# Kernel tuning notes

Hardware: AMD Instinct MI355X
Metric: run time of the kernel (lower is better)

Reference implementation:

```python
import jax, jax.numpy as jnp
import numpy as np

B, T, J, E, H = 32, 120, 24, 128, 8
d = E // H           # attention_dim = 16
D = J * E            # input_dim = 3072
FF = 256
NEG = -1e9


def _bn(x, g, b):
    # BatchNorm1d over channels-last layout: normalize each of D channels over (batch, time)
    m = x.mean(axis=(0, 1))
    v = x.var(axis=(0, 1))
    return (x - m) * jax.lax.rsqrt(v + 1e-5) * g + b


def setup_inputs() -> dict:
    key = jax.random.key(0)
    ks = jax.random.split(key, 12)
    s = 0.05  # keep activations well-scaled
    return {
        "src_seqs": jax.random.normal(ks[0], (B, T, D), jnp.float32),
        "Wq_t": jax.random.normal(ks[1], (H, J, d, E), jnp.float32) * s,
        "Wk_t": jax.random.normal(ks[2], (H, J, d, E), jnp.float32) * s,
        "Wv_t": jax.random.normal(ks[3], (H, J, d, E), jnp.float32) * s,
        "Wp_t": jax.random.normal(ks[4], (D, D), jnp.float32) * s,
        "bp_t": jnp.zeros((D,), jnp.float32),
        "g_t": jnp.ones((D,), jnp.float32),
        "b_t": jnp.zeros((D,), jnp.float32),
        "Wq_s": jax.random.normal(ks[5], (H, J, d, E), jnp.float32) * s,
        "Wk_s": jax.random.normal(ks[6], (H, d, E), jnp.float32) * s,
        "Wv_s": jax.random.normal(ks[7], (H, d, E), jnp.float32) * s,
        "Wp_s": jax.random.normal(ks[8], (D, D), jnp.float32) * s,
        "bp_s": jnp.zeros((D,), jnp.float32),
        "g_s": jnp.ones((D,), jnp.float32),
        "b_s": jnp.zeros((D,), jnp.float32),
        "W1": jax.random.normal(ks[9], (FF, D), jnp.float32) * s,
        "b1": jnp.zeros((FF,), jnp.float32),
        "W2": jax.random.normal(ks[10], (D, FF), jnp.float32) * s,
        "b2": jnp.zeros((D,), jnp.float32),
        "g_f": jnp.ones((D,), jnp.float32),
        "b_f": jnp.zeros((D,), jnp.float32),
    }


def reference(src_seqs, Wq_t, Wk_t, Wv_t, Wp_t, bp_t, g_t, b_t,
              Wq_s, Wk_s, Wv_s, Wp_s, bp_s, g_s, b_s,
              W1, b1, W2, b2, g_f, b_f):
    Bz, Tz, Dz = src_seqs.shape
    x = src_seqs.reshape(Bz, Tz, J, E)  # per-joint embeddings
    sc = 1.0 / jnp.sqrt(jnp.float32(d))

    # ---- temporal attention (per head h, per joint j; causal over time) ----
    q = jnp.einsum('btje,hjde->bhjtd', x, Wq_t)
    k = jnp.einsum('btje,hjde->bhjtd', x, Wk_t)
    v = jnp.einsum('btje,hjde->bhjtd', x, Wv_t)
    causal = jnp.where(jnp.tril(jnp.ones((Tz, Tz), bool)), 0.0, NEG)
    a = jax.nn.softmax(jnp.einsum('bhjtd,bhjsd->bhjts', q, k) * sc + causal, axis=-1)
    ta = jnp.einsum('bhjts,bhjsd->bhjtd', a, v)
    # concat order: heads outer, joints inner -> (b,t,h,j,d)
    ta = ta.transpose(0, 3, 1, 2, 4).reshape(Bz, Tz, Dz)
    ta = ta @ Wp_t.T + bp_t
    ta = _bn(ta + src_seqs, g_t, b_t)  # dropout=identity (eval)

    # ---- spatial attention (per head h; attends over joints, shared K/V proj) ----
    qs = jnp.einsum('btje,hjde->bhtjd', x, Wq_s)
    ks = jnp.einsum('btje,hde->bhtjd', x, Wk_s)
    vs = jnp.einsum('btje,hde->bhtjd', x, Wv_s)
    asft = jax.nn.softmax(jnp.einsum('bhtjd,bhtkd->bhtjk', qs, ks) * sc, axis=-1)
    sa = jnp.einsum('bhtjk,bhtkd->bhtjd', asft, vs)
    sa = sa.transpose(0, 2, 1, 3, 4).reshape(Bz, Tz, Dz)  # (b,t,h,j,d)
    sa = sa @ Wp_s.T + bp_s
    sa = _bn(sa + src_seqs, g_s, b_s)

    # ---- feed-forward + residual + norm ----
    att = ta + sa
    h1 = jax.nn.relu(att @ W1.T + b1)
    out = _bn((h1 @ W2.T + b2) + att, g_f, b_f)
    return out
```

## Files before the change

### kernel.cpp

```cpp
#include <hip/hip_runtime.h>

typedef unsigned short u16;
typedef __bf16 bf16x8 __attribute__((ext_vector_type(8)));
typedef float f4 __attribute__((ext_vector_type(4)));
typedef float float4v __attribute__((ext_vector_type(4)));
typedef u16 u16x4 __attribute__((ext_vector_type(4)));

#define NX 11796480
#define LDP 136

__device__ __forceinline__ float bf2f(u16 u){ __bf16 h = __builtin_bit_cast(__bf16, u); return (float)h; }
__device__ __forceinline__ u16 f2bf(float f){ __bf16 h = (__bf16)f; return __builtin_bit_cast(u16, h); }

__device__ __forceinline__ void gload_lds16(const u16* g, u16* l){
  __builtin_amdgcn_global_load_lds((const __attribute__((address_space(1))) void*)g,
                                   (__attribute__((address_space(3))) void*)l, 16, 0, 0);
}

__device__ __forceinline__ void cvt4seg(const float* __restrict__ in, u16* __restrict__ out, int i){
  float4v v = *(const float4v*)&in[i*4];
  u16x4 o;
  o[0]=f2bf(v[0]); o[1]=f2bf(v[1]); o[2]=f2bf(v[2]); o[3]=f2bf(v[3]);
  *(u16x4*)&out[i*4] = o;
}

__global__ void k_prep(const float* __restrict__ src, u16* __restrict__ x_bf,
                       const float* __restrict__ wpt, u16* __restrict__ wptb,
                       const float* __restrict__ wps, u16* __restrict__ wpsb,
                       const float* __restrict__ w1,  u16* __restrict__ w1b,
                       const float* __restrict__ w2,  u16* __restrict__ w2b,
                       const float* __restrict__ wqt, const float* __restrict__ wkt,
                       const float* __restrict__ wvt, const float* __restrict__ wqs,
                       const float* __restrict__ wks, const float* __restrict__ wvs,
                       u16* __restrict__ wcat, float* __restrict__ accs){
  int i = blockIdx.x*256 + threadIdx.x;
  if (i < 18432){ accs[i] = 0.f; return; }
  i -= 18432;
  if (i < 2949120){ cvt4seg(src, x_bf, i); return; }
  i -= 2949120;
  if (i < 2359296){ cvt4seg(wpt, wptb, i); return; }
  i -= 2359296;
  if (i < 2359296){ cvt4seg(wps, wpsb, i); return; }
  i -= 2359296;
  if (i < 196608){ cvt4seg(w1, w1b, i); return; }
  i -= 196608;
  if (i < 196608){ cvt4seg(w2, w2b, i); return; }
  i -= 196608;
  int e = i & 127;
  int n = (i >> 7) % 768;
  int j = i / (768*128);
  float v;
  if (n < 512){
    int tn = n >> 7, hh = (n >> 4) & 7, dd = n & 15;
    const float* W = (tn==0)? wqt : (tn==1)? wkt : (tn==2)? wvt : wqs;
    v = W[(((hh*24 + j)*16 + dd) << 7) + e];
  } else {
    int m = n - 512;
    int tn = m >> 7, hh = (m >> 4) & 7, dd = m & 15;
    const float* W = (tn==0)? wks : wvs;
    v = W[((hh*16 + dd) << 7) + e];
  }
  wcat[i] = f2bf(v);
}

__device__ __forceinline__ void stageQB(const u16* __restrict__ Bb, u16* __restrict__ dst,
                                        int tid, int srow16, int gcol){
  #pragma unroll
  for (int it=0; it<4; it++){
    int row = srow16 + it*16;
    gload_lds16(&Bb[(size_t)row*128 + gcol], dst + tid*8 + it*2048);
  }
}

__global__ __launch_bounds__(256)
void gemm_qkv(const u16* __restrict__ x, const u16* __restrict__ wcat,
              u16* __restrict__ qt, u16* __restrict__ kt, u16* __restrict__ vt,
              u16* __restrict__ qs, u16* __restrict__ ks, u16* __restrict__ vs)
{
  __shared__ __align__(16) u16 smem[32768];
  u16* As  = smem;
  u16* Bs0 = smem + 16384;
  u16* Bs1 = smem + 24576;
  int m0 = blockIdx.x*128, j = blockIdx.y;
  const u16* Ab = x + (size_t)m0*3072 + j*128;
  const u16* Bbase = wcat + (size_t)j*98304;
  int tid = threadIdx.x, lane = tid & 63, wid = tid >> 6;
  int quad = lane >> 4, r16 = lane & 15;
  int srow16 = tid >> 4;
  int cslot  = tid & 15;
  int gcol   = (cslot ^ srow16) * 8;

  #pragma unroll
  for (int it=0; it<8; it++){
    int row = srow16 + it*16;
    gload_lds16(&Ab[(size_t)row*3072 + gcol], As + tid*8 + it*2048);
  }
  stageQB(Bbase,            Bs0, tid, srow16, gcol);
  stageQB(Bbase + 64*128,   Bs1, tid, srow16, gcol);
  asm volatile("s_waitcnt vmcnt(4)" ::: "memory");
  __builtin_amdgcn_s_barrier();

  for (int nc=0; nc<12; nc++){
    const u16* Bc = (nc & 1) ? Bs1 : Bs0;

    f4 acc[2][4];
    #pragma unroll
    for (int mt=0; mt<2; mt++)
      #pragma unroll
      for (int nt=0; nt<4; nt++)
        #pragma unroll
        for (int q=0; q<4; q++) acc[mt][nt][q] = 0.f;

    #pragma unroll
    for (int kk=0; kk<4; kk++){
      const int soff = ((kk*4 + quad) ^ r16) * 8;
      bf16x8 af[2], bfr[4];
      #pragma unroll
      for (int mt=0; mt<2; mt++)
        af[mt] = *(const bf16x8*)&As[(wid*32 + mt*16 + r16)*128 + soff];
      #pragma unroll
      for (int nt=0; nt<4; nt++)
        bfr[nt] = *(const bf16x8*)&Bc[(nt*16 + r16)*128 + soff];
      #pragma unroll
      for (int mt=0; mt<2; mt++)
        #pragma unroll
        for (int nt=0; nt<4; nt++)
          acc[mt][nt] = __builtin_amdgcn_mfma_f32_16x16x32_bf16(af[mt], bfr[nt], acc[mt][nt], 0, 0, 0);
    }

    #pragma unroll
    for (int mt=0; mt<2; mt++){
      #pragma unroll
      for (int reg=0; reg<4; reg++){
        int row = m0 + wid*32 + mt*16 + quad*4 + reg;
        int b = row / 120, t = row % 120;
        #pragma unroll
        for (int nt=0; nt<4; nt++){
          int n = nc*64 + nt*16 + r16;
          u16 uv = f2bf(acc[mt][nt][reg]);
          if (n < 384){
            int tn = n >> 7, hh = (n >> 4) & 7, dd = n & 15;
            u16* base = (tn==0)? qt : (tn==1)? kt : vt;
            base[((((size_t)(b*8+hh)*24 + j)*120 + t) << 4) + dd] = uv;
          } else {
            int m2 = n - 384;
            int tn = m2 >> 7, hh = (m2 >> 4) & 7, dd = m2 & 15;
            u16* base = (tn==0)? qs : (tn==1)? ks : vs;
            base[((((size_t)row*8 + hh)*24 + j) << 4) + dd] = uv;
          }
        }
      }
    }

    if (nc < 11){
      __builtin_amdgcn_s_barrier();
      if (nc + 2 < 12){
        stageQB(Bbase + (size_t)(nc+2)*64*128, (nc & 1) ? Bs1 : Bs0, tid, srow16, gcol);
        asm volatile("s_waitcnt vmcnt(4)" ::: "memory");
      } else {
        asm volatile("s_waitcnt vmcnt(0)" ::: "memory");
      }
      __builtin_amdgcn_s_barrier();
    }
  }
}

__device__ __forceinline__ void stageA384(const u16* __restrict__ g, int kcol,
                                          u16* __restrict__ slotA, int lane, int wid){
  #pragma unroll
  for (int i=0;i<2;i++){
    int row = wid*32 + i*16 + (lane>>2);
    int sw  = (((lane & 3) ^ ((lane>>3) & 3)) << 3);
    gload_lds16(&g[(size_t)row*3072 + kcol + sw], slotA + (wid*2+i)*512);
  }
}
__device__ __forceinline__ void stageB384(const u16* __restrict__ g, int kcol,
                                          u16* __restrict__ slotB, int lane, int wid){
  #pragma unroll
  for (int i=0;i<3;i++){
    int row = wid*48 + i*16 + (lane>>2);
    int sw  = (((lane & 3) ^ ((lane>>3) & 3)) << 3);
    gload_lds16(&g[(size_t)row*3072 + kcol + sw], slotB + (wid*3+i)*512);
  }
}

__global__ __launch_bounds__(512, 2)
void gemm_proj384(const u16* __restrict__ A0, const u16* __restrict__ B0, const float* __restrict__ b0,
                  const u16* __restrict__ A1, const u16* __restrict__ B1, const float* __restrict__ b1v,
                  const u16* __restrict__ resb, u16* __restrict__ O0, u16* __restrict__ O1,
                  float* __restrict__ st0, float* __restrict__ st1)
{
  __shared__ __align__(16) u16 smem[61440];
  const int tid = threadIdx.x, lane = tid & 63, wid = tid >> 6;
  const int quad = lane >> 4, r16 = lane & 15;
  const int wm = wid >> 2, wn = wid & 3;

  int lin = blockIdx.x + 15*blockIdx.y + 120*blockIdx.z;
  int nidx = (lin & 7)*30 + (lin >> 3);
  int zz = nidx / 120; int rem = nidx - zz*120;
  int by = rem / 15, bx = rem - by*15;

  const int m0 = bx*256, n0 = by*384;
  const u16* Ag = (zz ? A1 : A0) + (size_t)m0*3072;
  const u16* Bg = (zz ? B1 : B0) + (size_t)n0*3072;
  const float* bias = zz ? b1v : b0;
  u16* out = zz ? O1 : O0;
  float* stp = zz ? st1 : st0;

  const int soff = ((quad ^ ((r16>>1)&3)) << 3);
  const int arow = wm*128 + r16;
  const int brow = wn*96 + r16;

  f4 acc[8][6];
  #pragma unroll
  for (int i=0;i<8;i++)
    #pragma unroll
    for (int n=0;n<6;n++)
      #pragma unroll
      for (int q=0;q<4;q++) acc[i][n][q] = 0.f;

  u16* Sa = smem;
  u16* Sb = smem + 20480;
  u16* Sc = smem + 40960;

  stageA384(Ag, 0,  Sa,        lane, wid);
  stageB384(Bg, 0,  Sa + 8192, lane, wid);
  stageA384(Ag, 32, Sb,        lane, wid);
  stageB384(Bg, 32, Sb + 8192, lane, wid);
  asm volatile("s_waitcnt vmcnt(5)" ::: "memory");
  __builtin_amdgcn_s_barrier();

  const int NT = 96;
  bf16x8 af[4], bf[6];

  for (int t=0; t<NT; ++t){
    const int kc2 = ((t+2 < NT) ? (t+2) : 0) * 32;

    #pragma unroll
    for (int i=0;i<4;i++) af[i] = *(const bf16x8*)&Sa[(arow + i*16)*32 + soff];
    #pragma unroll
    for (int n=0;n<6;n++) bf[n] = *(const bf16x8*)&Sa[8192 + (brow + n*16)*32 + soff];
    stageA384(Ag, kc2, Sc, lane, wid);
    __builtin_amdgcn_s_setprio(1);
    #pragma unroll
    for (int i=0;i<4;i++)
      #pragma unroll
      for (int n=0;n<6;n++)
        acc[i][n] = __builtin_amdgcn_mfma_f32_16x16x32_bf16(af[i], bf[n], acc[i][n], 0,0,0);
    __builtin_amdgcn_s_setprio(0);

    #pragma unroll
    for (int i=0;i<4;i++) af[i] = *(const bf16x8*)&Sa[(arow + 64 + i*16)*32 + soff];
    stageB384(Bg, kc2, Sc + 8192, lane, wid);
    __builtin_amdgcn_s_setprio(1);
    #pragma unroll
    for (int i=0;i<4;i++)
      #pragma unroll
      for (int n=0;n<6;n++)
        acc[4+i][n] = __builtin_amdgcn_mfma_f32_16x16x32_bf16(af[i], bf[n], acc[4+i][n], 0,0,0);
    __builtin_amdgcn_s_setprio(0);

    asm volatile("s_waitcnt vmcnt(5)" ::: "memory");
    __builtin_amdgcn_s_barrier();
    u16* tp = Sa; Sa = Sb; Sb = Sc; Sc = tp;
  }
  asm volatile("s_waitcnt vmcnt(0)" ::: "memory");

  float bv[6];
  #pragma unroll
  for (int n=0;n<6;n++) bv[n] = bias[n0 + wn*96 + n*16 + r16];
  float s[6] = {0,0,0,0,0,0}, s2[6] = {0,0,0,0,0,0};
  #pragma unroll
  for (int mf=0; mf<8; mf++){
    #pragma unroll
    for (int reg=0; reg<4; reg++){
      int grow = m0 + wm*128 + mf*16 + quad*4 + reg;
      #pragma unroll
      for (int n=0;n<6;n++){
        int gcol = n0 + wn*96 + n*16 + r16;
        size_t idx = (size_t)grow*3072 + gcol;
        float v = acc[mf][n][reg] + bv[n] + bf2f(resb[idx]);
        out[idx] = f2bf(v);
        s[n] += v; s2[n] += v*v;
      }
    }
  }
  #pragma unroll
  for (int n=0;n<6;n++){
    float a = s[n], b = s2[n];
    a += __shfl_xor(a, 16); a += __shfl_xor(a, 32);
    b += __shfl_xor(b, 16); b += __shfl_xor(b, 32);
    if (quad == 0){
      int col = n0 + wn*96 + n*16 + r16;
      atomicAdd(&stp[col], a);
      atomicAdd(&stp[3072 + col], b);
    }
  }
}

__device__ __forceinline__ void stageF(const u16* __restrict__ g, int k0,
                                       u16* __restrict__ dst, int wid, int srow, int gcol){
  #pragma unroll
  for (int i=0;i<4;i++){
    int row = srow + i*32;
    gload_lds16(&g[(size_t)row*256 + k0 + gcol], dst + wid*512 + i*2048);
  }
}

__global__ __launch_bounds__(256)
void gemm_ff2(const u16* __restrict__ A, const u16* __restrict__ B, const float* __restrict__ bias,
              const u16* __restrict__ resb, u16* __restrict__ out, float* __restrict__ stp)
{
  __shared__ __align__(16) u16 smem[32768];
  u16* Asb0 = smem;          u16* Asb1 = smem + 8192;
  u16* Bsb0 = smem + 16384;  u16* Bsb1 = smem + 24576;
  int m0 = blockIdx.x*128, n0 = blockIdx.y*128;
  const u16* Ag = A + (size_t)m0*256;
  const u16* Bg = B + (size_t)n0*256;
  int tid = threadIdx.x, lane = tid & 63, wid = tid >> 6;
  int quad = lane>>4, r16 = lane&15;
  int srow = tid >> 3;
  int gcol = ((tid & 7) ^ (srow & 7)) * 8;
  int waveM = (wid>>1)*64, waveN = (wid&1)*64;

  f4 acc[4][4];
  #pragma unroll
  for (int mt=0; mt<4; mt++)
    #pragma unroll
    for (int nt=0; nt<4; nt++)
      #pragma unroll
      for (int q=0; q<4; q++) acc[mt][nt][q] = 0.f;

  stageF(Ag, 0,  Asb0, wid, srow, gcol);
  stageF(Bg, 0,  Bsb0, wid, srow, gcol);
  stageF(Ag, 64, Asb1, wid, srow, gcol);
  stageF(Bg, 64, Bsb1, wid, srow, gcol);
  asm volatile("s_waitcnt vmcnt(8)" ::: "memory");
  __builtin_amdgcn_s_barrier();

  for (int t=0; t<4; t++){
    const u16* As = (t & 1) ? Asb1 : Asb0;
    const u16* Bs = (t & 1) ? Bsb1 : Bsb0;
    #pragma unroll
    for (int kk=0; kk<2; kk++){
      bf16x8 af[4], bfr[4];
      const int soff = ((kk*4 + quad) ^ (r16 & 7)) * 8;
      #pragma unroll
      for (int mt=0; mt<4; mt++)
        af[mt] = *(const bf16x8*)&As[(waveM + mt*16 + r16)*64 + soff];
      #pragma unroll
      for (int nt=0; nt<4; nt++)
        bfr[nt] = *(const bf16x8*)&Bs[(waveN + nt*16 + r16)*64 + soff];
      #pragma unroll
      for (int mt=0; mt<4; mt++)
        #pragma unroll
        for (int nt=0; nt<4; nt++)
          acc[mt][nt] = __builtin_amdgcn_mfma_f32_16x16x32_bf16(af[mt], bfr[nt], acc[mt][nt], 0, 0, 0);
    }
    if (t < 3){
      __builtin_amdgcn_s_barrier();
      if (t + 2 < 4){
        stageF(Ag, (t+2)*64, (t & 1) ? Asb1 : Asb0, wid, srow, gcol);
        stageF(Bg, (t+2)*64, (t & 1) ? Bsb1 : Bsb0, wid, srow, gcol);
        asm volatile("s_waitcnt vmcnt(8)" ::: "memory");
      } else {
        asm volatile("s_waitcnt vmcnt(0)" ::: "memory");
      }
      __builtin_amdgcn_s_barrier();
    }
  }

  float s[4] = {0,0,0,0}, s2[4] = {0,0,0,0};
  #pragma unroll
  for (int mt=0; mt<4; mt++){
    #pragma unroll
    for (int reg=0; reg<4; reg++){
      int grow = m0 + waveM + mt*16 + quad*4 + reg;
      #pragma unroll
      for (int nt=0; nt<4; nt++){
        int gcolo = n0 + waveN + nt*16 + r16;
        size_t idx = (size_t)grow*3072 + gcolo;
        float v = acc[mt][nt][reg] + bias[gcolo] + bf2f(resb[idx]);
        out[idx] = f2bf(v);
        s[nt] += v; s2[nt] += v*v;
      }
    }
  }
  #pragma unroll
  for (int nt=0; nt<4; nt++){
    float a = s[nt], b = s2[nt];
    a += __shfl_xor(a, 16); a += __shfl_xor(a, 32);
    b += __shfl_xor(b, 16); b += __shfl_xor(b, 32);
    if (quad == 0){
      int col = n0 + waveN + nt*16 + r16;
      atomicAdd(&stp[col], a);
      atomicAdd(&stp[3072 + col], b);
    }
  }
}

__device__ __forceinline__ void stageR_A(const u16* __restrict__ g, int kc, u16* __restrict__ slot,
                                         int tid, int srow, int gcol){
  gload_lds16(&g[(size_t)srow*3072 + kc + gcol], slot + tid*8);
}
__device__ __forceinline__ void stageR_B(const u16* __restrict__ g, int kc, u16* __restrict__ slot,
                                         int tid, int srow, int gcol){
  #pragma unroll
  for (int i=0;i<4;i++)
    gload_lds16(&g[(size_t)(srow + i*32)*3072 + kc + gcol], slot + 2048 + i*2048 + tid*8);
}

__global__ __launch_bounds__(256)
void gemm_relu(const u16* __restrict__ A, const u16* __restrict__ B,
               const float* __restrict__ bias, u16* __restrict__ out)
{
  __shared__ __align__(16) u16 smem[30720];
  const int tid = threadIdx.x, lane = tid & 63, wid = tid >> 6;
  const int quad = lane >> 4, r16 = lane & 15;
  const int waveM = (wid >> 1) * 16, waveN = (wid & 1) * 64;
  const int m0 = blockIdx.x * 32, n0 = blockIdx.y * 128;
  const u16* Ag = A + (size_t)m0 * 3072;
  const u16* Bg = B + (size_t)n0 * 3072;

  const int srow = tid >> 3;
  const int gcol = ((tid & 7) ^ (srow & 7)) * 8;

  f4 acc[4];
  #pragma unroll
  for (int n=0;n<4;n++)
    #pragma unroll
    for (int q=0;q<4;q++) acc[n][q] = 0.f;

  u16* Sa = smem;
  u16* Sb = smem + 10240;
  u16* Sc = smem + 20480;

  stageR_A(Ag, 0,  Sa, tid, srow, gcol);
  stageR_B(Bg, 0,  Sa, tid, srow, gcol);
  stageR_A(Ag, 64, Sb, tid, srow, gcol);
  stageR_B(Bg, 64, Sb, tid, srow, gcol);
  asm volatile("s_waitcnt vmcnt(5)" ::: "memory");
  __builtin_amdgcn_s_barrier();

  const int NT = 48;
  const int s0 = (quad ^ (r16 & 7)) * 8;
  const int s1 = ((4 + quad) ^ (r16 & 7)) * 8;

  for (int t=0; t<NT; ++t){
    const int kc2 = ((t+2 < NT) ? (t+2) : 0) * 64;

    bf16x8 a0 = *(const bf16x8*)&Sa[(waveM + r16)*64 + s0];
    bf16x8 b0[4];
    #pragma unroll
    for (int n=0;n<4;n++) b0[n] = *(const bf16x8*)&Sa[2048 + (waveN + n*16 + r16)*64 + s0];
    stageR_A(Ag, kc2, Sc, tid, srow, gcol);
    __builtin_amdgcn_s_setprio(1);
    #pragma unroll
    for (int n=0;n<4;n++)
      acc[n] = __builtin_amdgcn_mfma_f32_16x16x32_bf16(a0, b0[n], acc[n], 0,0,0);
    __builtin_amdgcn_s_setprio(0);

    bf16x8 a1 = *(const bf16x8*)&Sa[(waveM + r16)*64 + s1];
    bf16x8 b1[4];
    #pragma unroll
    for (int n=0;n<4;n++) b1[n] = *(const bf16x8*)&Sa[2048 + (waveN + n*16 + r16)*64 + s1];
    stageR_B(Bg, kc2, Sc, tid, srow, gcol);
    __builtin_amdgcn_s_setprio(1);
    #pragma unroll
    for (int n=0;n<4;n++)
      acc[n] = __builtin_amdgcn_mfma_f32_16x16x32_bf16(a1, b1[n], acc[n], 0,0,0);
    __builtin_amdgcn_s_setprio(0);

    asm volatile("s_waitcnt vmcnt(5)" ::: "memory");
    __builtin_amdgcn_s_barrier();
    u16* tp = Sa; Sa = Sb; Sb = Sc; Sc = tp;
  }
  asm volatile("s_waitcnt vmcnt(0)" ::: "memory");

  #pragma unroll
  for (int n=0;n<4;n++){
    int gcolo = n0 + waveN + n*16 + r16;
    float bv = bias[gcolo];
    #pragma unroll
    for (int reg=0; reg<4; reg++){
      int grow = m0 + waveM + quad*4 + reg;
      float v = acc[n][reg] + bv;
      out[(size_t)grow*256 + gcolo] = f2bf(v > 0.f ? v : 0.f);
    }
  }
}

__global__ __launch_bounds__(256)
void attn_both(const u16* __restrict__ qt, const u16* __restrict__ kt,
               const u16* __restrict__ vt, u16* __restrict__ ta,
               const u16* __restrict__ qsp, const u16* __restrict__ ksp,
               const u16* __restrict__ vsp, u16* __restrict__ sa)
{
  __shared__ __align__(16) char smem[39168];
  int tid = threadIdx.x, lane = tid & 63, wid = tid >> 6;
  int quad = lane >> 4, r16 = lane & 15;

  if (blockIdx.x < 6144){
    u16* P  = (u16*)smem;
    u16* Vt = (u16*)(smem + 34816);
    int blk = blockIdx.x;
    int b = blk / 192;
    int rem = blk % 192;
    int h = rem / 24, j = rem % 24;
    const u16* qb = qt + (size_t)blk*1920;
    const u16* kb = kt + (size_t)blk*1920;
    const u16* vb = vt + (size_t)blk*1920;

    if (tid < 240){
      int s = tid >> 1, hf = (tid & 1) * 8;
      bf16x8 vv = *(const bf16x8*)&vb[s*16 + hf];
      #pragma unroll
      for (int q=0;q<8;q++) Vt[(hf + q)*LDP + s] = __builtin_bit_cast(u16, (__bf16)vv[q]);
    }
    if (tid < 128){ int dd = tid >> 3, s = 120 + (tid & 7); Vt[dd*LDP + s] = 0; }
    __syncthreads();

    bf16x8 zv;
    #pragma unroll
    for (int i=0;i<8;i++) zv[i] = (__bf16)0.f;

    const int m0 = wid * 32;
    bf16x8 qf[2];
    #pragma unroll
    for (int mt=0; mt<2; mt++){
      int row = m0 + mt*16 + r16; if (row > 119) row = 119;
      qf[mt] = (quad < 2) ? *(const bf16x8*)&qb[row*16 + (quad&1)*8] : zv;
    }

    f4 S[2][8];
    #pragma unroll
    for (int nt=0; nt<8; nt++){
      int col = nt*16 + r16; int colc = col > 119 ? 119 : col;
      bf16x8 kf = (quad < 2) ? *(const bf16x8*)&kb[colc*16 + (quad&1)*8] : zv;
      #pragma unroll
      for (int mt=0; mt<2; mt++){
        f4 zz = {0.f, 0.f, 0.f, 0.f};
        S[mt][nt] = __builtin_amdgcn_mfma_f32_16x16x32_bf16(qf[mt], kf, zz, 0, 0, 0);
      }
    }

    #pragma unroll
    for (int mt=0; mt<2; mt++)
      #pragma unroll
      for (int nt=0; nt<8; nt++)
        #pragma unroll
        for (int reg=0; reg<4; reg++){
          int c = nt*16 + r16;
          int r = m0 + mt*16 + quad*4 + reg;
          float v = S[mt][nt][reg] * 0.25f;
          S[mt][nt][reg] = (c > r || c >= 120) ? -1e30f : v;
        }

    float Zr[2][4];
    #pragma unroll
    for (int mt=0; mt<2; mt++)
      #pragma unroll
      for (int reg=0; reg<4; reg++){
        float m = -1e30f;
        #pragma unroll
        for (int nt=0; nt<8; nt++) m = fmaxf(m, S[mt][nt][reg]);
        #pragma unroll
        for (int off=1; off<16; off<<=1) m = fmaxf(m, __shfl_xor(m, off, 16));
        float z = 0.f;
        #pragma unroll
        for (int nt=0; nt<8; nt++){
          float e = __expf(S[mt][nt][reg] - m);
          S[mt][nt][reg] = e;
          z += e;
        }
        #pragma unroll
        for (int off=1; off<16; off<<=1) z += __shfl_xor(z, off, 16);
        Zr[mt][reg] = z;
      }

    #pragma unroll
    for (int mt=0; mt<2; mt++)
      #pragma unroll
      for (int nt=0; nt<8; nt++)
        #pragma unroll
        for (int reg=0; reg<4; reg++)
          P[(m0 + mt*16 + quad*4 + reg)*LDP + nt*16 + r16] = f2bf(S[mt][nt][reg]);

    f4 O[2];
    #pragma unroll
    for (int mt=0; mt<2; mt++){ O[mt][0]=0.f; O[mt][1]=0.f; O[mt][2]=0.f; O[mt][3]=0.f; }
    #pragma unroll
    for (int kt8=0; kt8<4; kt8++){
      bf16x8 vf = *(const bf16x8*)&Vt[r16*LDP + kt8*32 + quad*8];
      #pragma unroll
      for (int mt=0; mt<2; mt++){
        bf16x8 pf = *(const bf16x8*)&P[(m0 + mt*16 + r16)*LDP + kt8*32 + quad*8];
        O[mt] = __builtin_amdgcn_mfma_f32_16x16x32_bf16(pf, vf, O[mt], 0, 0, 0);
      }
    }

    #pragma unroll
    for (int mt=0; mt<2; mt++)
      #pragma unroll
      for (int reg=0; reg<4; reg++){
        int r = m0 + mt*16 + quad*4 + reg;
        if (r < 120){
          size_t idx = (size_t)(b*120 + r)*3072 + h*384 + j*16 + r16;
          ta[idx] = f2bf(O[mt][reg] / Zr[mt][reg]);
        }
      }
  } else {
    float* Ks = (float*)smem;
    float* Vs = (float*)(smem + 12288);
    int bt = blockIdx.x - 6144;
    size_t base = (size_t)bt * 3072;
    for (int c = tid; c < 384; c += 256){
      bf16x8 kv = *(const bf16x8*)&ksp[base + c*8];
      bf16x8 vv = *(const bf16x8*)&vsp[base + c*8];
      #pragma unroll
      for (int i=0;i<8;i++){ Ks[c*8+i] = (float)kv[i]; Vs[c*8+i] = (float)vv[i]; }
    }
    __syncthreads();
    if (tid < 192){
      int h = tid / 24, j = tid % 24;
      float q[16];
      #pragma unroll
      for (int d2=0; d2<16; d2++) q[d2] = bf2f(qsp[base + h*384 + j*16 + d2]);
      float sc[24], mx = -1e30f;
      #pragma unroll
      for (int kk=0; kk<24; kk++){
        float dot = 0.f;
        #pragma unroll
        for (int d2=0; d2<16; d2++) dot += q[d2]*Ks[h*384 + kk*16 + d2];
        sc[kk] = dot * 0.25f;
        mx = fmaxf(mx, sc[kk]);
      }
      float Z = 0.f, acc[16];
      #pragma unroll
      for (int d2=0; d2<16; d2++) acc[d2] = 0.f;
      #pragma unroll
      for (int kk=0; kk<24; kk++){
        float w = __expf(sc[kk] - mx);
        Z += w;
        #pragma unroll
        for (int d2=0; d2<16; d2++) acc[d2] += w*Vs[h*384 + kk*16 + d2];
      }
      float inv = 1.f / Z;
      #pragma unroll
      for (int d2=0; d2<16; d2++) sa[base + h*384 + j*16 + d2] = f2bf(acc[d2]*inv);
    }
  }
}

__global__ void bn_coef2(const float* __restrict__ accT, const float* __restrict__ gT,
                         const float* __restrict__ bT, float* __restrict__ cT,
                         const float* __restrict__ accS, const float* __restrict__ gS,
                         const float* __restrict__ bS, float* __restrict__ cS){
  int isS = blockIdx.x >= 12;
  const float* acc = isS ? accS : accT;
  const float* g   = isS ? gS : gT;
  const float* b   = isS ? bS : bT;
  float* coef      = isS ? cS : cT;
  int c = (blockIdx.x % 12)*256 + threadIdx.x;
  float mean = acc[c] * (1.f/3840.f);
  float var  = acc[3072+c] * (1.f/3840.f) - mean*mean;
  float sc = g[c] * rsqrtf(var + 1e-5f);
  coef[c] = sc;
  coef[3072+c] = b[c] - mean*sc;
}

__global__ void bn_coef(const float* __restrict__ acc, const float* __restrict__ g,
                        const float* __restrict__ b, float* __restrict__ coef){
  int c = blockIdx.x*256 + threadIdx.x;
  float mean = acc[c] * (1.f/3840.f);
  float var  = acc[3072+c] * (1.f/3840.f) - mean*mean;
  float sc = g[c] * rsqrtf(var + 1e-5f);
  coef[c] = sc;
  coef[3072+c] = b[c] - mean*sc;
}

__global__ void bn_apply2(const u16* __restrict__ Ytb, const u16* __restrict__ Ysb,
                          const float* __restrict__ ct, const float* __restrict__ cs,
                          u16* __restrict__ attB){
  int i = blockIdx.x*256 + threadIdx.x;
  int c = (i*4) % 3072;
  u16x4 yt = *(const u16x4*)&Ytb[i*4];
  u16x4 ys = *(const u16x4*)&Ysb[i*4];
  u16x4 o;
  #pragma unroll
  for (int k=0;k<4;k++){
    float a = bf2f(yt[k])*ct[c+k] + ct[3072+c+k] + bf2f(ys[k])*cs[c+k] + cs[3072+c+k];
    o[k] = f2bf(a);
  }
  *(u16x4*)&attB[i*4] = o;
}

__global__ void bn_out(const u16* __restrict__ Yfb, const float* __restrict__ cf,
                       float* __restrict__ out){
  int i = blockIdx.x*256 + threadIdx.x;
  int c = (i*4) % 3072;
  u16x4 yf = *(const u16x4*)&Yfb[i*4];
  float4v o;
  #pragma unroll
  for (int k=0;k<4;k++) o[k] = bf2f(yf[k])*cf[c+k] + cf[3072+c+k];
  *(float4v*)&out[i*4] = o;
}

extern "C" void kernel_launch(void* const* d_in, const int* in_sizes, int n_in,
                              void* d_out, int out_size, void* d_ws, size_t ws_size,
                              hipStream_t stream)
{
  const float* src  = (const float*)d_in[0];
  const float* Wq_t = (const float*)d_in[1];
  const float* Wk_t = (const float*)d_in[2];
  const float* Wv_t = (const float*)d_in[3];
  const float* Wp_t = (const float*)d_in[4];
  const float* bp_t = (const float*)d_in[5];
  const float* g_t  = (const float*)d_in[6];
  const float* b_t  = (const float*)d_in[7];
  const float* Wq_s = (const float*)d_in[8];
  const float* Wk_s = (const float*)d_in[9];
  const float* Wv_s = (const float*)d_in[10];
  const float* Wp_s = (const float*)d_in[11];
  const float* bp_s = (const float*)d_in[12];
  const float* g_s  = (const float*)d_in[13];
  const float* b_s  = (const float*)d_in[14];
  const float* W1   = (const float*)d_in[15];
  const float* b1   = (const float*)d_in[16];
  const float* W2   = (const float*)d_in[17];
  const float* b2   = (const float*)d_in[18];
  const float* g_f  = (const float*)d_in[19];
  const float* b_f  = (const float*)d_in[20];

  char* ws = (char*)d_ws;
  u16* x_bf  = (u16*)(ws + 0ull);
  u16* wptb  = (u16*)(ws + 23592960ull);
  u16* wpsb  = (u16*)(ws + 42467328ull);
  u16* w1b   = (u16*)(ws + 61341696ull);
  u16* w2b   = (u16*)(ws + 62914560ull);
  u16* wcat  = (u16*)(ws + 64487424ull);
  u16* qt    = (u16*)(ws + 69206016ull);
  u16* kt    = qt + NX;
  u16* vt    = kt + NX;
  u16* qs    = vt + NX;
  u16* ks    = qs + NX;
  u16* vs    = ks + NX;
  u16* tab   = (u16*)(ws + 210763776ull);
  u16* sab   = (u16*)(ws + 234356736ull);
  float* accT = (float*)(ws + 257949696ull);
  float* accS = accT + 6144;
  float* accF = accS + 6144;
  float* cT   = accF + 6144;
  float* cS   = cT + 6144;
  float* cF   = cS + 6144;
  u16* Ytb  = qt;
  u16* Ysb  = kt;
  u16* attB = vt;
  u16* Yfb  = qs;
  u16* h1   = wcat;
  float* out = (float*)d_out;

  k_prep<<<40776, 256, 0, stream>>>(src, x_bf, Wp_t, wptb, Wp_s, wpsb, W1, w1b, W2, w2b,
                                    Wq_t, Wk_t, Wv_t, Wq_s, Wk_s, Wv_s, wcat, accT);
  gemm_qkv<<<dim3(30,24), 256, 0, stream>>>(x_bf, wcat, qt, kt, vt, qs, ks, vs);
  attn_both<<<9984, 256, 0, stream>>>(qt, kt, vt, tab, qs, ks, vs, sab);
  gemm_proj384<<<dim3(15,8,2), 512, 0, stream>>>(tab, wptb, bp_t, sab, wpsb, bp_s,
                                                 x_bf, Ytb, Ysb, accT, accS);
  bn_coef2<<<24, 256, 0, stream>>>(accT, g_t, b_t, cT, accS, g_s, b_s, cS);
  bn_apply2<<<11520, 256, 0, stream>>>(Ytb, Ysb, cT, cS, attB);
  gemm_relu<<<dim3(120,2), 256, 0, stream>>>(attB, w1b, b1, h1);
  gemm_ff2<<<dim3(30,24), 256, 0, stream>>>(h1, w2b, b2, attB, Yfb, accF);
  bn_coef<<<12, 256, 0, stream>>>(accF, g_f, b_f, cF);
  bn_out<<<11520, 256, 0, stream>>>(Yfb, cF, out);
}
```

Before: 554.9 us.

## Stage QKV GEMM output through LDS for vectorized scattered stores

The QKV projection epilogue now writes each 128x64 accumulator tile to a new LDS buffer, then re-reads it so each thread emits 8-byte vector stores into the q/k/v layouts, replacing per-element 2-byte scattered stores. The spatial q/k/v layout changes to (row, j, h, d), matching the GEMM's natural column order, and the spatial attention kernel's indexing is updated to read it. This costs extra LDS (80KB total), an additional barrier per chunk, and adjusted vmcnt waits to account for the outstanding stores.

New measurement: 519.6 us. 6.3% less time.

```diff
diff --git a/kernel.cpp b/kernel.cpp
--- a/kernel.cpp
+++ b/kernel.cpp
@@ -77,18 +77,18 @@
               u16* __restrict__ qt, u16* __restrict__ kt, u16* __restrict__ vt,
               u16* __restrict__ qs, u16* __restrict__ ks, u16* __restrict__ vs)
 {
-  __shared__ __align__(16) u16 smem[32768];
+  __shared__ __align__(16) u16 smem[40960];
   u16* As  = smem;
   u16* Bs0 = smem + 16384;
   u16* Bs1 = smem + 24576;
+  u16* Ct  = smem + 32768;
   int m0 = blockIdx.x*128, j = blockIdx.y;
   const u16* Ab = x + (size_t)m0*3072 + j*128;
   const u16* Bbase = wcat + (size_t)j*98304;
   int tid = threadIdx.x, lane = tid & 63, wid = tid >> 6;
   int quad = lane >> 4, r16 = lane & 15;
   int srow16 = tid >> 4;
-  int cslot  = tid & 15;
-  int gcol   = (cslot ^ srow16) * 8;
+  int gcol   = ((tid & 15) ^ srow16) * 8;
 
   #pragma unroll
   for (int it=0; it<8; it++){
@@ -100,6 +100,10 @@
   asm volatile("s_waitcnt vmcnt(4)" ::: "memory");
   __builtin_amdgcn_s_barrier();
 
+  const int c0 = (tid & 15) * 4;
+  const int hl = c0 >> 4;
+  const int d0 = c0 & 15;
+
   for (int nc=0; nc<12; nc++){
     const u16* Bc = (nc & 1) ? Bs1 : Bs0;
 
@@ -129,36 +133,48 @@
     }
 
     #pragma unroll
-    for (int mt=0; mt<2; mt++){
+    for (int mt=0; mt<2; mt++)
       #pragma unroll
       for (int reg=0; reg<4; reg++){
-        int row = m0 + wid*32 + mt*16 + quad*4 + reg;
-        int b = row / 120, t = row % 120;
-        #pragma unroll
-        for (int nt=0; nt<4; nt++){
-          int n = nc*64 + nt*16 + r16;
-          u16 uv = f2bf(acc[mt][nt][reg]);
-          if (n < 384){
-            int tn = n >> 7, hh = (n >> 4) & 7, dd = n & 15;
-            u16* base = (tn==0)? qt : (tn==1)? kt : vt;
-            base[((((size_t)(b*8+hh)*24 + j)*120 + t) << 4) + dd] = uv;
-          } else {
-            int m2 = n - 384;
-            int tn = m2 >> 7, hh = (m2 >> 4) & 7, dd = m2 & 15;
-            u16* base = (tn==0)? qs : (tn==1)? ks : vs;
-            base[((((size_t)row*8 + hh)*24 + j) << 4) + dd] = uv;
-          }
-        }
+        int row = wid*32 + mt*16 + quad*4 + reg;
+        #pragma unroll
+        for (int nt=0; nt<4; nt++)
+          Ct[row*64 + nt*16 + r16] = f2bf(acc[mt][nt][reg]);
+      }
+    asm volatile("s_waitcnt lgkmcnt(0)" ::: "memory");
+    __builtin_amdgcn_s_barrier();
+
+    if (nc < 6){
+      int tn = nc >> 1;
+      u16* base = (tn==0)? qt : (tn==1)? kt : vt;
+      int hh = (nc & 1)*4 + hl;
+      #pragma unroll
+      for (int g=0; g<8; g++){
+        int row = g*16 + (tid >> 4);
+        int gr = m0 + row;
+        int b = gr / 120, t = gr - b*120;
+        u16x4 v = *(const u16x4*)&Ct[row*64 + c0];
+        *(u16x4*)&base[((((size_t)(b*8+hh)*24 + j)*120 + t) << 4) + d0] = v;
+      }
+    } else {
+      int tn = (nc - 6) >> 1;
+      u16* base = (tn==0)? qs : (tn==1)? ks : vs;
+      int hh = ((nc - 6) & 1)*4 + hl;
+      #pragma unroll
+      for (int g=0; g<8; g++){
+        int row = g*16 + (tid >> 4);
+        size_t gr = (size_t)(m0 + row);
+        u16x4 v = *(const u16x4*)&Ct[row*64 + c0];
+        *(u16x4*)&base[gr*3072 + j*128 + hh*16 + d0] = v;
       }
     }
 
     if (nc < 11){
-      __builtin_amdgcn_s_barrier();
       if (nc + 2 < 12){
         stageQB(Bbase + (size_t)(nc+2)*64*128, (nc & 1) ? Bs1 : Bs0, tid, srow16, gcol);
-        asm volatile("s_waitcnt vmcnt(4)" ::: "memory");
+        asm volatile("s_waitcnt vmcnt(12)" ::: "memory");
       } else {
-        asm volatile("s_waitcnt vmcnt(0)" ::: "memory");
+        asm volatile("s_waitcnt vmcnt(8)" ::: "memory");
       }
       __builtin_amdgcn_s_barrier();
     }
@@ -625,13 +641,13 @@
       int h = tid / 24, j = tid % 24;
       float q[16];
       #pragma unroll
-      for (int d2=0; d2<16; d2++) q[d2] = bf2f(qsp[base + h*384 + j*16 + d2]);
+      for (int d2=0; d2<16; d2++) q[d2] = bf2f(qsp[base + j*128 + h*16 + d2]);
       float sc[24], mx = -1e30f;
       #pragma unroll
       for (int kk=0; kk<24; kk++){
         float dot = 0.f;
         #pragma unroll
-        for (int d2=0; d2<16; d2++) dot += q[d2]*Ks[h*384 + kk*16 + d2];
+        for (int d2=0; d2<16; d2++) dot += q[d2]*Ks[kk*128 + h*16 + d2];
         sc[kk] = dot * 0.25f;
         mx = fmaxf(mx, sc[kk]);
       }
@@ -643,7 +659,7 @@
         float w = __expf(sc[kk] - mx);
         Z += w;
         #pragma unroll
-        for (int d2=0; d2<16; d2++) acc[d2] += w*Vs[h*384 + kk*16 + d2];
+        for (int d2=0; d2<16; d2++) acc[d2] += w*Vs[kk*128 + h*16 + d2];
       }
       float inv = 1.f / Z;
       #pragma unroll
```
